# Performance work log

Hardware: AMD Instinct MI355X
Metric: run time of the kernel (lower is better)

## Reference

```python
import jax, jax.numpy as jnp
import numpy as np

P_DIMS = [512, 256, 128]
K_DIMS = [256, 256, 256]
NT = 65536


def setup_inputs() -> dict:
    key = jax.random.key(0)
    ks = jax.random.split(key, 8 * len(P_DIMS))
    inp = {}
    ki = 0
    for i, (p, k) in enumerate(zip(P_DIMS, K_DIMS)):
        inp[f"x{i}"] = jax.random.normal(ks[ki], (NT, p), jnp.float32); ki += 1
        inp[f"alpha{i}"] = jax.random.normal(ks[ki], (1, k), jnp.float32); ki += 1
        inp[f"beta{i}"] = jax.random.normal(ks[ki], (k, p), jnp.float32) * 0.05; ki += 1
        inp[f"sig{i}"] = jax.random.normal(ks[ki], (1, k), jnp.float32); ki += 1
        inp[f"eta{i}"] = jax.random.normal(ks[ki], (1, k), jnp.float32); ki += 1
        inp[f"gam{i}"] = jax.random.normal(ks[ki], (k, 1), jnp.float32) * 0.03; ki += 1
        inp[f"w{i}"] = jax.random.normal(ks[ki], (k, p), jnp.float32); ki += 1
        inp[f"disc{i}"] = jnp.array([3.0], jnp.float32); ki += 1
    return inp


def _source(x, alpha, beta, sig, eta, gam, w, disc):
    # x: (nt,p); w,beta: (k,p); alpha,sig,eta: (1,k); gam: (k,1); disc: (1,)
    h = eta ** 2                                           # (1,k)
    d2 = (jnp.sum(x * x, axis=1, keepdims=True)
          - 2.0 * (x @ w.T)
          + jnp.sum(w * w, axis=1)[None, :])
    a = jnp.exp(-(gam[:, 0] ** 2)[None, :] * d2)           # (nt,k)
    ah = a * h                                             # a * H
    hx = jnp.sum(ah, axis=1)                               # (nt,)
    mu = x @ beta.T + alpha                                # (nt,k)
    mux = jnp.sum(mu * ah, axis=1) / hx
    sig2x = jnp.sum((sig ** 2) * (ah ** 2), axis=1) / (hx * hx)
    hx_dc = hx * jax.nn.sigmoid(disc[0])
    return mux, sig2x, hx, hx_dc


def reference(x0, alpha0, beta0, sig0, eta0, gam0, w0, disc0,
              x1, alpha1, beta1, sig1, eta1, gam1, w1, disc1,
              x2, alpha2, beta2, sig2, eta2, gam2, w2, disc2):
    srcs = [
        (x0, alpha0, beta0, sig0, eta0, gam0, w0, disc0),
        (x1, alpha1, beta1, sig1, eta1, gam1, w1, disc1),
        (x2, alpha2, beta2, sig2, eta2, gam2, w2, disc2),
    ]
    outs = [_source(*s) for s in srcs]  # fixed small loop over sources
    mux_t = jnp.stack([o[0] for o in outs])     # (S,nt)
    sig2x_t = jnp.stack([o[1] for o in outs])
    hx_t = jnp.stack([o[2] for o in outs])
    hx_dc = jnp.stack([o[3] for o in outs])
    denom = jnp.sum(hx_dc, axis=0)
    mux_comb = jnp.sum(mux_t * hx_dc, axis=0) / denom
    sig2x_comb = jnp.sum(sig2x_t * hx_dc ** 2, axis=0) / (denom ** 2)
    mux_final = jnp.concatenate([mux_t, mux_comb[None]], axis=0)      # (S+1,nt)
    sig2x_final = jnp.concatenate([sig2x_t, sig2x_comb[None]], axis=0)
    hx_final = jnp.concatenate([hx_t, denom[None]], axis=0)
    return (mux_final, sig2x_final, hx_final)
```

## Files before the change

kernel.cpp:

```cpp
#include <hip/hip_runtime.h>
#include <hip/hip_bf16.h>

typedef __attribute__((ext_vector_type(8))) short short8;
typedef __attribute__((ext_vector_type(4))) float f32x4;

#define NT 65536

__device__ __forceinline__ unsigned short f2bf(float f) {
    union { float f; unsigned int u; } v; v.f = f;
    unsigned int u = v.u;
    unsigned int r = (u + 0x7fffu + ((u >> 16) & 1u)) >> 16;
    return (unsigned short)r;
}

__device__ __forceinline__ unsigned int cvt_pk_bf16(float lo, float hi) {
    unsigned int r;
    asm("v_cvt_pk_bf16_f32 %0, %1, %2" : "=v"(r) : "v"(lo), "v"(hi));
    return r;
}

#define LGKM0()  asm volatile("s_waitcnt lgkmcnt(0)" ::: "memory")
#define BAR()    __builtin_amdgcn_s_barrier()
#define SB0()    __builtin_amdgcn_sched_barrier(0)

__global__ void prep_kernel(const float* __restrict__ w0, const float* __restrict__ b0,
                            const float* __restrict__ a0, const float* __restrict__ s0,
                            const float* __restrict__ e0, const float* __restrict__ g0,
                            const float* __restrict__ w1, const float* __restrict__ b1,
                            const float* __restrict__ a1, const float* __restrict__ s1,
                            const float* __restrict__ e1, const float* __restrict__ g1,
                            const float* __restrict__ w2, const float* __restrict__ b2,
                            const float* __restrict__ a2, const float* __restrict__ s2,
                            const float* __restrict__ e2, const float* __restrict__ g2,
                            unsigned short* __restrict__ bc, float* __restrict__ prmAll) {
    __shared__ float red[2];
    const int bx = blockIdx.x;
    const int s = bx >> 9;
    const int n = bx & 511;
    const int P = 512 >> s;
    const float* w   = (s == 0) ? w0 : ((s == 1) ? w1 : w2);
    const float* bet = (s == 0) ? b0 : ((s == 1) ? b1 : b2);
    const float* alp = (s == 0) ? a0 : ((s == 1) ? a1 : a2);
    const float* sig = (s == 0) ? s0 : ((s == 1) ? s1 : s2);
    const float* eta = (s == 0) ? e0 : ((s == 1) ? e1 : e2);
    const float* gam = (s == 0) ? g0 : ((s == 1) ? g1 : g2);
    unsigned short* dstb = bc + ((s == 0) ? 0 : ((s == 1) ? (512 * 512) : (512 * 512 + 512 * 256)));
    float* prm = prmAll + 1280 * s;

    const int tid = threadIdx.x;
    const int k16 = n >> 5;
    const int typ = (n >> 4) & 1;
    const int k = k16 * 16 + (n & 15);
    const bool isw = (typ == 0);
    const float* src = (isw ? w : bet) + (size_t)k * P;
    unsigned short* dst = dstb + (size_t)n * P;
    float ss = 0.f;
    for (int c = tid; c < P; c += 128) {
        float f = src[c];
        dst[c] = f2bf(f);
        if (isw) ss += f * f;
    }
#pragma unroll
    for (int m = 1; m < 64; m <<= 1) ss += __shfl_xor(ss, m);
    if ((tid & 63) == 0) red[tid >> 6] = ss;
    __syncthreads();
    if (isw && tid == 0) prm[k] = red[0] + red[1];
    if (n == 0) {
        for (int kk = tid; kk < 256; kk += 128) {
            float g = gam[kk], e = eta[kk];
            prm[256 + kk]  = g * g;
            prm[512 + kk]  = e * e;
            prm[768 + kk]  = alp[kk];
            prm[1024 + kk] = sig[kk] * sig[kk];
        }
    }
}

template<int P>
__global__ __launch_bounds__(512, 2)
void fused_src(const float* __restrict__ x, const unsigned short* __restrict__ Bc,
               const float* __restrict__ prm, float* __restrict__ pwsS) {
    constexpr int KSW = P / 32;
    constexpr int CPT = P / 64;
    constexpr int QPT = (CPT / 2 > 0) ? CPT / 2 : 1;
    constexpr int T = 8;

    __shared__ unsigned short Xs[2][32 * P];
    __shared__ float xn2[2][32];
    __shared__ float part[8][32][3];

    const int b = blockIdx.x;
    const int h = b >> 8;
    const int rg = b & 255;
    const int rowbase = rg * 256;

    const int tid = threadIdx.x, lane = tid & 63, wv = tid >> 6;
    const int l15 = lane & 15, l4 = lane >> 4;
    const int k16 = h * 8 + wv;

    const int srow = tid >> 4;
    const int sc = tid & 15;
    const float* xth = x + (size_t)(rowbase + srow) * P + sc * (P / 16);

    short8 Bf0[KSW], Bf1[KSW];
#pragma unroll
    for (int ks = 0; ks < KSW; ks++) {
        Bf0[ks] = *(const short8*)(Bc + (size_t)(k16 * 32 + l15) * P + ks * 32 + l4 * 8);
        Bf1[ks] = *(const short8*)(Bc + (size_t)(k16 * 32 + 16 + l15) * P + ks * 32 + l4 * 8);
    }

    f32x4 acc00 = {0,0,0,0}, acc01 = {0,0,0,0}, acc10 = {0,0,0,0}, acc11 = {0,0,0,0};
    float4 xr[CPT];

    auto issueX = [&](int t) {
#pragma unroll
        for (int j = 0; j < CPT; j++)
            xr[j] = *(const float4*)(xth + (size_t)t * 32 * P + j * 4);
    };
    auto cvtWrite = [&](int bufp) {
        float s = 0.f;
#pragma unroll
        for (int q = 0; q < QPT; q++) {
            float4 a = xr[2 * q], c = xr[2 * q + 1];
            s += a.x*a.x + a.y*a.y + a.z*a.z + a.w*a.w
               + c.x*c.x + c.y*c.y + c.z*c.z + c.w*c.w;
            uint4 pk = { cvt_pk_bf16(a.x, a.y), cvt_pk_bf16(a.z, a.w),
                         cvt_pk_bf16(c.x, c.y), cvt_pk_bf16(c.z, c.w) };
            const int m = sc * QPT + q;
            *(uint4*)(&Xs[bufp][srow * P + ((m ^ (srow & 7)) << 3)]) = pk;
        }
        s += __shfl_xor(s, 1); s += __shfl_xor(s, 2);
        s += __shfl_xor(s, 4); s += __shfl_xor(s, 8);
        if (sc == 0) xn2[bufp][srow] = s;
    };
    auto compute = [&](int bufp) {
#pragma unroll
        for (int ks = 0; ks < KSW; ks++) {
            const int m = (ks * 4 + l4) ^ (l15 & 7);
            short8 xf0 = *(const short8*)(&Xs[bufp][l15 * P + (m << 3)]);
            short8 xf1 = *(const short8*)(&Xs[bufp][(16 + l15) * P + (m << 3)]);
            acc00 = __builtin_amdgcn_mfma_f32_16x16x32_bf16(Bf0[ks], xf0, acc00, 0, 0, 0);
            acc10 = __builtin_amdgcn_mfma_f32_16x16x32_bf16(Bf1[ks], xf0, acc10, 0, 0, 0);
            acc01 = __builtin_amdgcn_mfma_f32_16x16x32_bf16(Bf0[ks], xf1, acc01, 0, 0, 0);
            acc11 = __builtin_amdgcn_mfma_f32_16x16x32_bf16(Bf1[ks], xf1, acc11, 0, 0, 0);
        }
    };

    issueX(0); SB0();
    cvtWrite(0); SB0();
    issueX(1); SB0();

#pragma unroll
    for (int t = 0; t < T; t++) {
        LGKM0(); SB0(); BAR(); SB0();
        if (t + 1 < T) { cvtWrite((t + 1) & 1); SB0(); }
        if (t + 2 < T) { issueX(t + 2); SB0(); }
        compute(t & 1);
        SB0();

        {
            const int kb = k16 * 16 + 4 * l4;
            const f32x4 wn2 = *(const f32x4*)(prm + kb);
            const f32x4 g2  = *(const f32x4*)(prm + 256 + kb);
            const f32x4 hv  = *(const f32x4*)(prm + 512 + kb);
            const f32x4 alv = *(const f32x4*)(prm + 768 + kb);
            const f32x4 s2v = *(const f32x4*)(prm + 1024 + kb);
#pragma unroll
            for (int xf = 0; xf < 2; xf++) {
                const int xrow = xf * 16 + l15;
                const float xv = xn2[t & 1][xrow];
                const f32x4 aw = xf ? acc01 : acc00;
                const f32x4 ab = xf ? acc11 : acc10;
                float hs = 0.f, ms = 0.f, gs = 0.f;
#pragma unroll
                for (int j = 0; j < 4; j++) {
                    const float d2 = xv - 2.f * aw[j] + wn2[j];
                    const float e  = __expf(-g2[j] * d2);
                    const float ah = e * hv[j];
                    hs += ah;
                    ms += (ab[j] + alv[j]) * ah;
                    gs += s2v[j] * ah * ah;
                }
                hs += __shfl_xor(hs, 16); hs += __shfl_xor(hs, 32);
                ms += __shfl_xor(ms, 16); ms += __shfl_xor(ms, 32);
                gs += __shfl_xor(gs, 16); gs += __shfl_xor(gs, 32);
                if (l4 == 0) {
                    part[wv][xrow][0] = hs;
                    part[wv][xrow][1] = ms;
                    part[wv][xrow][2] = gs;
                }
            }
        }
        LGKM0(); SB0(); BAR(); SB0();
        if (tid < 96) {
            const int v = tid >> 5, r = tid & 31;
            float s = 0.f;
#pragma unroll
            for (int w8 = 0; w8 < 8; w8++) s += part[w8][r][v];
            pwsS[(size_t)(h * 3 + v) * NT + rowbase + t * 32 + r] = s;
        }
        acc00 = (f32x4){0,0,0,0}; acc01 = (f32x4){0,0,0,0};
        acc10 = (f32x4){0,0,0,0}; acc11 = (f32x4){0,0,0,0};
    }
}

__global__ void combine_kernel(const float* __restrict__ pws,
                               const float* __restrict__ d0, const float* __restrict__ d1,
                               const float* __restrict__ d2, float* __restrict__ out) {
    const int t = blockIdx.x * 256 + threadIdx.x;
    float mux[3], s2x[3], hx[3];
#pragma unroll
    for (int s = 0; s < 3; s++) {
        const float* bb = pws + (size_t)s * 6 * NT;
        const float hh = bb[t] + bb[(size_t)3 * NT + t];
        const float mm = bb[(size_t)1 * NT + t] + bb[(size_t)4 * NT + t];
        const float gg = bb[(size_t)2 * NT + t] + bb[(size_t)5 * NT + t];
        mux[s] = mm / hh; s2x[s] = gg / (hh * hh); hx[s] = hh;
        out[(size_t)s * NT + t]       = mux[s];
        out[(size_t)(4 + s) * NT + t] = s2x[s];
        out[(size_t)(8 + s) * NT + t] = hh;
    }
    const float sd0 = 1.f / (1.f + __expf(-d0[0]));
    const float sd1 = 1.f / (1.f + __expf(-d1[0]));
    const float sd2 = 1.f / (1.f + __expf(-d2[0]));
    const float c0 = hx[0] * sd0, c1 = hx[1] * sd1, c2 = hx[2] * sd2;
    const float den = c0 + c1 + c2;
    const float muc = mux[0] * c0 + mux[1] * c1 + mux[2] * c2;
    const float sgc = s2x[0] * c0 * c0 + s2x[1] * c1 * c1 + s2x[2] * c2 * c2;
    out[(size_t)3 * NT + t]  = muc / den;
    out[(size_t)7 * NT + t]  = sgc / (den * den);
    out[(size_t)11 * NT + t] = den;
}

extern "C" void kernel_launch(void* const* d_in, const int* in_sizes, int n_in,
                              void* d_out, int out_size, void* d_ws, size_t ws_size,
                              hipStream_t stream) {
    const float* x0 = (const float*)d_in[0];
    const float* x1 = (const float*)d_in[8];
    const float* x2 = (const float*)d_in[16];

    unsigned short* bc = (unsigned short*)d_ws;
    float* prmAll = (float*)((char*)d_ws + 917504);
    float* pws    = (float*)((char*)d_ws + 917504 + 15360);
    float* out = (float*)d_out;

    prep_kernel<<<1536, 128, 0, stream>>>(
        (const float*)d_in[6],  (const float*)d_in[2],  (const float*)d_in[1],
        (const float*)d_in[3],  (const float*)d_in[4],  (const float*)d_in[5],
        (const float*)d_in[14], (const float*)d_in[10], (const float*)d_in[9],
        (const float*)d_in[11], (const float*)d_in[12], (const float*)d_in[13],
        (const float*)d_in[22], (const float*)d_in[18], (const float*)d_in[17],
        (const float*)d_in[19], (const float*)d_in[20], (const float*)d_in[21],
        bc, prmAll);

    const size_t bcoff1 = 512 * 512, bcoff2 = 512 * 512 + 512 * 256;
    fused_src<512><<<512, 512, 0, stream>>>(x0, bc,          prmAll,        pws);
    fused_src<256><<<512, 512, 0, stream>>>(x1, bc + bcoff1, prmAll + 1280, pws + (size_t)6 * NT);
    fused_src<128><<<512, 512, 0, stream>>>(x2, bc + bcoff2, prmAll + 2560, pws + (size_t)12 * NT);
    combine_kernel<<<256, 256, 0, stream>>>(pws, (const float*)d_in[7], (const float*)d_in[15],
                                            (const float*)d_in[23], out);
}
```

Before: 148.7 us.

## Merge per-source kernels into one 256x256-tiled K-streaming GEMM kernel

Replaces the three per-source launches with one 1536-block kernel that dispatches on block index to a templated body. Each block now computes a 256-row by 256-column tile of the bf16 weight block, streaming K in 32-wide slices with triple-buffered LDS staging of both x and weights, instead of holding a 32-row weight slice in registers per wave. The intent is to remove launch gaps between sources, keep each weight fragment in use across many more rows, and run the heavy MFMA tile at higher priority. The cost is large accumulator register pressure (32 f32x4 per thread) with 2 blocks per SM requested, and the exp/reduction epilogue now runs once after the K loop, which may cause spills or lower occupancy.

```diff
diff --git a/kernel.cpp b/kernel.cpp
--- a/kernel.cpp
+++ b/kernel.cpp
@@ -77,131 +77,164 @@
 }
 
 template<int P>
+__device__ __forceinline__ void body(const float* __restrict__ x,
+                                     const unsigned short* __restrict__ Bc,
+                                     const float* __restrict__ prm,
+                                     float* __restrict__ pwsS, int h, int mt,
+                                     unsigned short (*As)[256 * 40], unsigned short (*Xs)[256 * 40],
+                                     float* xn2, float (*part)[256][3], int tid) {
+    constexpr int NK = P / 32;
+    const int lane = tid & 63, wv = tid >> 6;
+    const int wr = wv >> 2, wc = wv & 3;
+    const int l15 = lane & 15, l4 = lane >> 4;
+    const int row0 = mt * 256;
+
+    const int rx = tid >> 1, hx = tid & 1;
+    const float* xp = x + (size_t)(row0 + rx) * P + hx * 16;
+    const unsigned short* ap = Bc + (size_t)(256 * h + rx) * P + hx * 16;
+
+    f32x4 acc[8][4];
+#pragma unroll
+    for (int m = 0; m < 8; m++)
+#pragma unroll
+        for (int nf = 0; nf < 4; nf++) acc[m][nf] = (f32x4){0.f, 0.f, 0.f, 0.f};
+
+    float4 xr[3][4];
+    uint4  ar[3][2];
+    float ssx = 0.f;
+    short8 Bfr[4];
+
+    auto issue = [&](int set, int t) {
+#pragma unroll
+        for (int j = 0; j < 4; j++) xr[set][j] = *(const float4*)(xp + t * 32 + j * 4);
+#pragma unroll
+        for (int q = 0; q < 2; q++) ar[set][q] = *(const uint4*)(ap + t * 32 + q * 8);
+    };
+    auto stage = [&](int set, int buf) {
+#pragma unroll
+        for (int q = 0; q < 2; q++) {
+            float4 a = xr[set][2 * q], b = xr[set][2 * q + 1];
+            ssx += a.x*a.x + a.y*a.y + a.z*a.z + a.w*a.w
+                 + b.x*b.x + b.y*b.y + b.z*b.z + b.w*b.w;
+            uint4 pk = { cvt_pk_bf16(a.x, a.y), cvt_pk_bf16(a.z, a.w),
+                         cvt_pk_bf16(b.x, b.y), cvt_pk_bf16(b.z, b.w) };
+            *(uint4*)(&Xs[buf][rx * 40 + (hx * 2 + q) * 8]) = pk;
+        }
+#pragma unroll
+        for (int q = 0; q < 2; q++)
+            *(uint4*)(&As[buf][rx * 40 + (hx * 2 + q) * 8]) = ar[set][q];
+    };
+    auto compute = [&](int buf) {
+#pragma unroll
+        for (int mh = 0; mh < 2; mh++) {
+            short8 Af[4];
+            if (mh == 0) {
+#pragma unroll
+                for (int nf = 0; nf < 4; nf++)
+                    Bfr[nf] = *(const short8*)(&Xs[buf][(wc * 64 + nf * 16 + l15) * 40 + l4 * 8]);
+            }
+#pragma unroll
+            for (int i = 0; i < 4; i++)
+                Af[i] = *(const short8*)(&As[buf][(wr * 128 + (mh * 4 + i) * 16 + l15) * 40 + l4 * 8]);
+            SB0();
+            __builtin_amdgcn_s_setprio(1);
+#pragma unroll
+            for (int i = 0; i < 4; i++)
+#pragma unroll
+                for (int nf = 0; nf < 4; nf++)
+                    acc[mh * 4 + i][nf] = __builtin_amdgcn_mfma_f32_16x16x32_bf16(
+                        Af[i], Bfr[nf], acc[mh * 4 + i][nf], 0, 0, 0);
+            __builtin_amdgcn_s_setprio(0);
+            SB0();
+        }
+    };
+
+    issue(0, 0); SB0();
+    issue(1, 1); SB0();
+    stage(0, 0);
+    issue(2, 2); SB0();
+    LGKM0(); BAR(); SB0();
+
+#pragma unroll
+    for (int t = 0; t < NK; t++) {
+        if (t + 1 < NK) { stage((t + 1) % 3, (t + 1) % 3); SB0(); }
+        if (t + 3 < NK) { issue((t + 3) % 3, t + 3); SB0(); }
+        compute(t % 3);
+        LGKM0(); SB0(); BAR(); SB0();
+    }
+
+    ssx += __shfl_xor(ssx, 1);
+    if (hx == 0) xn2[rx] = ssx;
+    __syncthreads();
+
+    f32x4 wn2[4], g2[4], hv[4], alv[4], s2v[4];
+#pragma unroll
+    for (int g = 0; g < 4; g++) {
+        const int kb = (h * 8 + wr * 4 + g) * 16 + 4 * l4;
+        wn2[g] = *(const f32x4*)(prm + kb);
+        g2[g]  = *(const f32x4*)(prm + 256 + kb);
+        hv[g]  = *(const f32x4*)(prm + 512 + kb);
+        alv[g] = *(const f32x4*)(prm + 768 + kb);
+        s2v[g] = *(const f32x4*)(prm + 1024 + kb);
+    }
+#pragma unroll
+    for (int nf = 0; nf < 4; nf++) {
+        const int col = wc * 64 + nf * 16 + l15;
+        const float xv = xn2[col];
+        float hs = 0.f, ms = 0.f, gs = 0.f;
+#pragma unroll
+        for (int g = 0; g < 4; g++) {
+#pragma unroll
+            for (int j = 0; j < 4; j++) {
+                const float aw = acc[2 * g][nf][j];
+                const float ab = acc[2 * g + 1][nf][j];
+                const float d2 = xv - 2.f * aw + wn2[g][j];
+                const float e  = __expf(-g2[g][j] * d2);
+                const float ah = e * hv[g][j];
+                hs += ah;
+                ms += (ab + alv[g][j]) * ah;
+                gs += s2v[g][j] * ah * ah;
+            }
+        }
+        hs += __shfl_xor(hs, 16); hs += __shfl_xor(hs, 32);
+        ms += __shfl_xor(ms, 16); ms += __shfl_xor(ms, 32);
+        gs += __shfl_xor(gs, 16); gs += __shfl_xor(gs, 32);
+        if (l4 == 0) {
+            part[wr][col][0] = hs;
+            part[wr][col][1] = ms;
+            part[wr][col][2] = gs;
+        }
+    }
+    __syncthreads();
+    if (tid < 256) {
+#pragma unroll
+        for (int v = 0; v < 3; v++)
+            pwsS[(size_t)(h * 3 + v) * NT + row0 + tid] = part[0][tid][v] + part[1][tid][v];
+    }
+}
+
 __global__ __launch_bounds__(512, 2)
-void fused_src(const float* __restrict__ x, const unsigned short* __restrict__ Bc,
-               const float* __restrict__ prm, float* __restrict__ pwsS) {
-    constexpr int KSW = P / 32;
-    constexpr int CPT = P / 64;
-    constexpr int QPT = (CPT / 2 > 0) ? CPT / 2 : 1;
-    constexpr int T = 8;
-
-    __shared__ unsigned short Xs[2][32 * P];
-    __shared__ float xn2[2][32];
-    __shared__ float part[8][32][3];
-
-    const int b = blockIdx.x;
-    const int h = b >> 8;
-    const int rg = b & 255;
-    const int rowbase = rg * 256;
-
-    const int tid = threadIdx.x, lane = tid & 63, wv = tid >> 6;
-    const int l15 = lane & 15, l4 = lane >> 4;
-    const int k16 = h * 8 + wv;
-
-    const int srow = tid >> 4;
-    const int sc = tid & 15;
-    const float* xth = x + (size_t)(rowbase + srow) * P + sc * (P / 16);
-
-    short8 Bf0[KSW], Bf1[KSW];
-#pragma unroll
-    for (int ks = 0; ks < KSW; ks++) {
-        Bf0[ks] = *(const short8*)(Bc + (size_t)(k16 * 32 + l15) * P + ks * 32 + l4 * 8);
-        Bf1[ks] = *(const short8*)(Bc + (size_t)(k16 * 32 + 16 + l15) * P + ks * 32 + l4 * 8);
-    }
-
-    f32x4 acc00 = {0,0,0,0}, acc01 = {0,0,0,0}, acc10 = {0,0,0,0}, acc11 = {0,0,0,0};
-    float4 xr[CPT];
-
-    auto issueX = [&](int t) {
-#pragma unroll
-        for (int j = 0; j < CPT; j++)
-            xr[j] = *(const float4*)(xth + (size_t)t * 32 * P + j * 4);
-    };
-    auto cvtWrite = [&](int bufp) {
-        float s = 0.f;
-#pragma unroll
-        for (int q = 0; q < QPT; q++) {
-            float4 a = xr[2 * q], c = xr[2 * q + 1];
-            s += a.x*a.x + a.y*a.y + a.z*a.z + a.w*a.w
-               + c.x*c.x + c.y*c.y + c.z*c.z + c.w*c.w;
-            uint4 pk = { cvt_pk_bf16(a.x, a.y), cvt_pk_bf16(a.z, a.w),
-                         cvt_pk_bf16(c.x, c.y), cvt_pk_bf16(c.z, c.w) };
-            const int m = sc * QPT + q;
-            *(uint4*)(&Xs[bufp][srow * P + ((m ^ (srow & 7)) << 3)]) = pk;
-        }
-        s += __shfl_xor(s, 1); s += __shfl_xor(s, 2);
-        s += __shfl_xor(s, 4); s += __shfl_xor(s, 8);
-        if (sc == 0) xn2[bufp][srow] = s;
-    };
-    auto compute = [&](int bufp) {
-#pragma unroll
-        for (int ks = 0; ks < KSW; ks++) {
-            const int m = (ks * 4 + l4) ^ (l15 & 7);
-            short8 xf0 = *(const short8*)(&Xs[bufp][l15 * P + (m << 3)]);
-            short8 xf1 = *(const short8*)(&Xs[bufp][(16 + l15) * P + (m << 3)]);
-            acc00 = __builtin_amdgcn_mfma_f32_16x16x32_bf16(Bf0[ks], xf0, acc00, 0, 0, 0);
-            acc10 = __builtin_amdgcn_mfma_f32_16x16x32_bf16(Bf1[ks], xf0, acc10, 0, 0, 0);
-            acc01 = __builtin_amdgcn_mfma_f32_16x16x32_bf16(Bf0[ks], xf1, acc01, 0, 0, 0);
-            acc11 = __builtin_amdgcn_mfma_f32_16x16x32_bf16(Bf1[ks], xf1, acc11, 0, 0, 0);
-        }
-    };
-
-    issueX(0); SB0();
-    cvtWrite(0); SB0();
-    issueX(1); SB0();
-
-#pragma unroll
-    for (int t = 0; t < T; t++) {
-        LGKM0(); SB0(); BAR(); SB0();
-        if (t + 1 < T) { cvtWrite((t + 1) & 1); SB0(); }
-        if (t + 2 < T) { issueX(t + 2); SB0(); }
-        compute(t & 1);
-        SB0();
-
-        {
-            const int kb = k16 * 16 + 4 * l4;
-            const f32x4 wn2 = *(const f32x4*)(prm + kb);
-            const f32x4 g2  = *(const f32x4*)(prm + 256 + kb);
-            const f32x4 hv  = *(const f32x4*)(prm + 512 + kb);
-            const f32x4 alv = *(const f32x4*)(prm + 768 + kb);
-            const f32x4 s2v = *(const f32x4*)(prm + 1024 + kb);
-#pragma unroll
-            for (int xf = 0; xf < 2; xf++) {
-                const int xrow = xf * 16 + l15;
-                const float xv = xn2[t & 1][xrow];
-                const f32x4 aw = xf ? acc01 : acc00;
-                const f32x4 ab = xf ? acc11 : acc10;
-                float hs = 0.f, ms = 0.f, gs = 0.f;
-#pragma unroll
-                for (int j = 0; j < 4; j++) {
-                    const float d2 = xv - 2.f * aw[j] + wn2[j];
-                    const float e  = __expf(-g2[j] * d2);
-                    const float ah = e * hv[j];
-                    hs += ah;
-                    ms += (ab[j] + alv[j]) * ah;
-                    gs += s2v[j] * ah * ah;
-                }
-                hs += __shfl_xor(hs, 16); hs += __shfl_xor(hs, 32);
-                ms += __shfl_xor(ms, 16); ms += __shfl_xor(ms, 32);
-                gs += __shfl_xor(gs, 16); gs += __shfl_xor(gs, 32);
-                if (l4 == 0) {
-                    part[wv][xrow][0] = hs;
-                    part[wv][xrow][1] = ms;
-                    part[wv][xrow][2] = gs;
-                }
-            }
-        }
-        LGKM0(); SB0(); BAR(); SB0();
-        if (tid < 96) {
-            const int v = tid >> 5, r = tid & 31;
-            float s = 0.f;
-#pragma unroll
-            for (int w8 = 0; w8 < 8; w8++) s += part[w8][r][v];
-            pwsS[(size_t)(h * 3 + v) * NT + rowbase + t * 32 + r] = s;
-        }
-        acc00 = (f32x4){0,0,0,0}; acc01 = (f32x4){0,0,0,0};
-        acc10 = (f32x4){0,0,0,0}; acc11 = (f32x4){0,0,0,0};
-    }
+void fused_all(const float* __restrict__ x0, const float* __restrict__ x1, const float* __restrict__ x2,
+               const unsigned short* __restrict__ bcAll, const float* __restrict__ prmAll,
+               float* __restrict__ pws) {
+    __shared__ unsigned short As[3][256 * 40];
+    __shared__ unsigned short Xs[3][256 * 40];
+    __shared__ float xn2[256];
+    __shared__ float part[2][256][3];
+
+    const int bx = blockIdx.x;
+    const int src = bx >> 9;
+    const int local = bx & 511;
+    const int h = local >> 8;
+    const int mt = local & 255;
+    const int tid = threadIdx.x;
+
+    if (src == 0)
+        body<512>(x0, bcAll, prmAll, pws, h, mt, As, Xs, xn2, part, tid);
+    else if (src == 1)
+        body<256>(x1, bcAll + 512 * 512, prmAll + 1280, pws + (size_t)6 * NT, h, mt, As, Xs, xn2, part, tid);
+    else
+        body<128>(x2, bcAll + 512 * 512 + 512 * 256, prmAll + 2560, pws + (size_t)12 * NT, h, mt, As, Xs, xn2, part, tid);
 }
 
 __global__ void combine_kernel(const float* __restrict__ pws,
@@ -253,10 +286,7 @@
         (const float*)d_in[19], (const float*)d_in[20], (const float*)d_in[21],
         bc, prmAll);
 
-    const size_t bcoff1 = 512 * 512, bcoff2 = 512 * 512 + 512 * 256;
-    fused_src<512><<<512, 512, 0, stream>>>(x0, bc,          prmAll,        pws);
-    fused_src<256><<<512, 512, 0, stream>>>(x1, bc + bcoff1, prmAll + 1280, pws + (size_t)6 * NT);
-    fused_src<128><<<512, 512, 0, stream>>>(x2, bc + bcoff2, prmAll + 2560, pws + (size_t)12 * NT);
+    fused_all<<<1536, 512, 0, stream>>>(x0, x1, x2, bc, prmAll, pws);
     combine_kernel<<<256, 256, 0, stream>>>(pws, (const float*)d_in[7], (const float*)d_in[15],
                                             (const float*)d_in[23], out);
 }
```

Measured after the change: 161.6 us. +8.7%, slower.
